# Optimization experiments

Measured on AMD Instinct MI355X. Metric: run time of the kernel, lower is better.

## Reference

```python
import jax, jax.numpy as jnp
import numpy as np

def setup_inputs() -> dict:
    key = jax.random.key(0)
    k1, k2, k3 = jax.random.split(key, 3)
    input_dim, hidden_dim = 512, 1024
    batch, seq_len = 32, 1024
    fan_in = input_dim + hidden_dim
    bound = 1.0 / np.sqrt(fan_in)
    x = jax.random.normal(k1, (batch, seq_len, input_dim), dtype=jnp.float32)
    # nn.Linear(input_dim+hidden_dim, 4*hidden_dim): weight [4H, I+H], bias [4H]
    W = jax.random.uniform(k2, (4 * hidden_dim, fan_in), minval=-bound, maxval=bound, dtype=jnp.float32)
    b = jax.random.uniform(k3, (4 * hidden_dim,), minval=-bound, maxval=bound, dtype=jnp.float32)
    return {"x": x, "W": W, "b": b}

def reference(x, W, b):
    B, T, I = x.shape
    H4 = W.shape[0]
    H = H4 // 4
    # Split weight into input and hidden parts (concat(x, h) @ W.T == x @ Wx.T + h @ Wh.T)
    Wx = W[:, :I]   # [4H, I]
    Wh = W[:, I:]   # [4H, H]
    # Precompute input contribution for all timesteps in one GEMM
    xW = jnp.einsum('bti,gi->btg', x, Wx) + b  # [B, T, 4H]

    def step(carry, xw_t):
        h, c = carry
        gates = xw_t + h @ Wh.T  # [B, 4H]
        i_t, f_t, g_t, o_t = jnp.split(gates, 4, axis=1)
        i_t = jax.nn.sigmoid(i_t)
        f_t = jax.nn.sigmoid(f_t)
        g_t = jnp.tanh(g_t)
        o_t = jax.nn.sigmoid(o_t)
        c_new = f_t * c + i_t * g_t
        h_new = o_t * jnp.tanh(c_new)
        return (h_new, c_new), h_new

    h0 = jnp.zeros((B, H), dtype=x.dtype)
    c0 = jnp.zeros((B, H), dtype=x.dtype)
    (_, _), hs = jax.lax.scan(step, (h0, c0), jnp.swapaxes(xW, 0, 1))  # hs: [T, B, H]
    return jnp.swapaxes(hs, 0, 1)  # [B, T, H]
```

## Files before the change

kernel.cpp:

```cpp
#include <hip/hip_runtime.h>
#include <cstdint>

#define BB 32
#define TT 1024
#define II 512
#define HH 1024
#define NTHREADS 512
#define NBLOCKS  256

__device__ __forceinline__ float sigm(float v) { return 1.0f / (1.0f + __expf(-v)); }
__device__ __forceinline__ float mytanh(float v) {
  float e = __expf(2.0f * v);
  return (e - 1.0f) / (e + 1.0f);
}

__global__ __launch_bounds__(NTHREADS, 2)
void lstm_step(const float* __restrict__ x, const float* __restrict__ W,
               const float* __restrict__ bias, const float* __restrict__ h_in,
               float* __restrict__ h_out, float* __restrict__ c_state,
               float* __restrict__ out, int t)
{
  __shared__ __align__(16) float sm[BB * HH];
  const int tid   = threadIdx.x;
  const int wave  = tid >> 6;
  const int lane  = tid & 63;
  const int ul    = wave >> 1;
  const int u     = blockIdx.x * 4 + ul;
  const int bbase = (wave & 1) * 16;

  float wreg[4][24];
  float bias4[4];
  #pragma unroll
  for (int q = 0; q < 4; ++q) {
    const float* wr = W + (size_t)(q * HH + u) * (II + HH);
    #pragma unroll
    for (int j = 0; j < 24; ++j) wreg[q][j] = wr[lane + 64 * j];
    bias4[q] = bias[q * HH + u];
  }

  float acc[16][4];
  #pragma unroll
  for (int bl = 0; bl < 16; ++bl)
    #pragma unroll
    for (int q = 0; q < 4; ++q) acc[bl][q] = 0.0f;

  for (int idx = tid; idx < BB * II / 4; idx += NTHREADS) {
    const int b  = idx >> 7;
    const int ii = idx & 127;
    reinterpret_cast<float4*>(sm)[idx] =
        reinterpret_cast<const float4*>(x + (size_t)b * TT * II + (size_t)t * II)[ii];
  }
  __syncthreads();

  #pragma unroll
  for (int bl = 0; bl < 16; ++bl) {
    const float* row = sm + (bbase + bl) * II;
    float xv[8];
    #pragma unroll
    for (int j = 0; j < 8; ++j) xv[j] = row[lane + 64 * j];
    #pragma unroll
    for (int q = 0; q < 4; ++q)
      #pragma unroll
      for (int j = 0; j < 8; ++j) acc[bl][q] = fmaf(xv[j], wreg[q][j], acc[bl][q]);
  }
  __syncthreads();

  for (int idx = tid; idx < BB * HH / 4; idx += NTHREADS)
    reinterpret_cast<float4*>(sm)[idx] = reinterpret_cast<const float4*>(h_in)[idx];
  __syncthreads();

  #pragma unroll
  for (int bl = 0; bl < 16; ++bl) {
    const float* row = sm + (bbase + bl) * HH;
    float hv[16];
    #pragma unroll
    for (int j = 0; j < 16; ++j) hv[j] = row[lane + 64 * j];
    #pragma unroll
    for (int q = 0; q < 4; ++q)
      #pragma unroll
      for (int j = 0; j < 16; ++j) acc[bl][q] = fmaf(hv[j], wreg[q][8 + j], acc[bl][q]);
  }

  float g4[4] = {0.f, 0.f, 0.f, 0.f};
  #pragma unroll
  for (int bl = 0; bl < 16; ++bl) {
    float a0 = acc[bl][0], a1 = acc[bl][1], a2 = acc[bl][2], a3 = acc[bl][3];
    #pragma unroll
    for (int off = 32; off; off >>= 1) {
      a0 += __shfl_xor(a0, off, 64);
      a1 += __shfl_xor(a1, off, 64);
      a2 += __shfl_xor(a2, off, 64);
      a3 += __shfl_xor(a3, off, 64);
    }
    if (lane == bl) { g4[0] = a0; g4[1] = a1; g4[2] = a2; g4[3] = a3; }
  }

  if (lane < 16) {
    const int b = bbase + lane;
    const float gi = sigm(g4[0] + bias4[0]);
    const float gf = sigm(g4[1] + bias4[1]);
    const float gg = mytanh(g4[2] + bias4[2]);
    const float go = sigm(g4[3] + bias4[3]);
    const int ci = b * HH + u;
    const float cn = gf * c_state[ci] + gi * gg;
    c_state[ci] = cn;
    const float hn = go * mytanh(cn);
    h_out[ci] = hn;
    out[(size_t)b * TT * HH + (size_t)t * HH + u] = hn;
  }
}

extern "C" void kernel_launch(void* const* d_in, const int* in_sizes, int n_in,
                              void* d_out, int out_size, void* d_ws, size_t ws_size,
                              hipStream_t stream)
{
  const float* x = (const float*)d_in[0];
  const float* W = (const float*)d_in[1];
  const float* b = (const float*)d_in[2];
  float* out = (float*)d_out;

  float* h0 = (float*)d_ws;
  float* h1 = h0 + BB * HH;
  float* c  = h1 + BB * HH;
  hipMemsetAsync(d_ws, 0, (size_t)3 * BB * HH * sizeof(float), stream);

  for (int t = 0; t < TT; ++t) {
    const float* hin = (t & 1) ? h1 : h0;
    float*      hout = (t & 1) ? h0 : h1;
    lstm_step<<<NBLOCKS, NTHREADS, 0, stream>>>(x, W, b, hin, hout, c, out, t);
  }
}
```

Before: 24.24 ms.

## Replace per-timestep launches with persistent cooperative kernel using grid barrier

Turns the 1024 separate step launches into one cooperative persistent kernel. Blocks synchronise through a global atomic barrier between timesteps and keep weights and the cell state in registers. The previous h is read back from the output tensor into LDS with direct global-to-LDS loads, double-buffered with the next x slice. A transpose-style shuffle reduction has each lane hold one gate, removing the per-batch reduction loops. This removes launch overhead and weight reloads per step, at the cost of a spin barrier and a dependence on all 256 blocks being co-resident.

```diff
diff --git a/kernel.cpp b/kernel.cpp
--- a/kernel.cpp
+++ b/kernel.cpp
@@ -5,108 +5,186 @@
 #define TT 1024
 #define II 512
 #define HH 1024
+#define KK 1536
 #define NTHREADS 512
 #define NBLOCKS  256
 
-__device__ __forceinline__ float sigm(float v) { return 1.0f / (1.0f + __expf(-v)); }
-__device__ __forceinline__ float mytanh(float v) {
-  float e = __expf(2.0f * v);
-  return (e - 1.0f) / (e + 1.0f);
+__device__ __forceinline__ void gload16(const void* g, void* l) {
+  __builtin_amdgcn_global_load_lds(
+      (const __attribute__((address_space(1))) unsigned int*)g,
+      (__attribute__((address_space(3))) unsigned int*)l, 16, 0, 0);
+}
+
+__device__ __forceinline__ void grid_barrier(unsigned* bar) {
+  __syncthreads();
+  if (threadIdx.x == 0) {
+    __threadfence();
+    unsigned g = __hip_atomic_load(bar + 1, __ATOMIC_RELAXED, __HIP_MEMORY_SCOPE_AGENT);
+    unsigned old = __hip_atomic_fetch_add(bar, 1u, __ATOMIC_ACQ_REL, __HIP_MEMORY_SCOPE_AGENT);
+    if (old == NBLOCKS - 1) {
+      __hip_atomic_store(bar, 0u, __ATOMIC_RELAXED, __HIP_MEMORY_SCOPE_AGENT);
+      __hip_atomic_fetch_add(bar + 1, 1u, __ATOMIC_RELEASE, __HIP_MEMORY_SCOPE_AGENT);
+    } else {
+      while (__hip_atomic_load(bar + 1, __ATOMIC_ACQUIRE, __HIP_MEMORY_SCOPE_AGENT) == g)
+        __builtin_amdgcn_s_sleep(1);
+    }
+    __threadfence();
+  }
+  __syncthreads();
 }
 
 __global__ __launch_bounds__(NTHREADS, 2)
-void lstm_step(const float* __restrict__ x, const float* __restrict__ W,
-               const float* __restrict__ bias, const float* __restrict__ h_in,
-               float* __restrict__ h_out, float* __restrict__ c_state,
-               float* __restrict__ out, int t)
+void lstm_persist(const float* __restrict__ x, const float* __restrict__ W,
+                  const float* __restrict__ bias, float* __restrict__ out,
+                  unsigned* __restrict__ bar)
 {
-  __shared__ __align__(16) float sm[BB * HH];
+  __shared__ __align__(16) float smA[BB * II];
+  __shared__ __align__(16) float smB[BB * II];
+
   const int tid   = threadIdx.x;
+  const int lane  = tid & 63;
   const int wave  = tid >> 6;
-  const int lane  = tid & 63;
-  const int ul    = wave >> 1;
-  const int u     = blockIdx.x * 4 + ul;
+  const int u     = blockIdx.x * 4 + (wave >> 1);
   const int bbase = (wave & 1) * 16;
-
-  float wreg[4][24];
-  float bias4[4];
+  const int g4    = lane >> 2;
+  const int q     = lane & 3;
+
+  float wr[4][24];
   #pragma unroll
-  for (int q = 0; q < 4; ++q) {
-    const float* wr = W + (size_t)(q * HH + u) * (II + HH);
-    #pragma unroll
-    for (int j = 0; j < 24; ++j) wreg[q][j] = wr[lane + 64 * j];
-    bias4[q] = bias[q * HH + u];
-  }
-
-  float acc[16][4];
+  for (int r = 0; r < 4; ++r) {
+    const int qq = q ^ r;
+    const float* row = W + (size_t)(qq * HH + u) * KK;
+    #pragma unroll
+    for (int j = 0; j < 2; ++j) {
+      float4 v = *(const float4*)(row + 4 * lane + 256 * j);
+      wr[r][4*j+0] = v.x; wr[r][4*j+1] = v.y; wr[r][4*j+2] = v.z; wr[r][4*j+3] = v.w;
+    }
+    #pragma unroll
+    for (int j = 0; j < 4; ++j) {
+      float4 v = *(const float4*)(row + 512 + 4 * lane + 256 * j);
+      wr[r][8+4*j+0] = v.x; wr[r][8+4*j+1] = v.y; wr[r][8+4*j+2] = v.z; wr[r][8+4*j+3] = v.w;
+    }
+  }
+  const float bmine = bias[q * HH + u];
+  float c_reg = 0.0f;
+
   #pragma unroll
-  for (int bl = 0; bl < 16; ++bl)
-    #pragma unroll
-    for (int q = 0; q < 4; ++q) acc[bl][q] = 0.0f;
-
-  for (int idx = tid; idx < BB * II / 4; idx += NTHREADS) {
-    const int b  = idx >> 7;
-    const int ii = idx & 127;
-    reinterpret_cast<float4*>(sm)[idx] =
-        reinterpret_cast<const float4*>(x + (size_t)b * TT * II + (size_t)t * II)[ii];
+  for (int it = 0; it < 8; ++it) {
+    int idx = it * NTHREADS + tid;
+    int b = idx >> 7, c4 = idx & 127;
+    gload16(x + (size_t)b * TT * II + 4 * c4, smA + 4 * idx);
   }
   __syncthreads();
 
-  #pragma unroll
-  for (int bl = 0; bl < 16; ++bl) {
-    const float* row = sm + (bbase + bl) * II;
-    float xv[8];
-    #pragma unroll
-    for (int j = 0; j < 8; ++j) xv[j] = row[lane + 64 * j];
-    #pragma unroll
-    for (int q = 0; q < 4; ++q)
-      #pragma unroll
-      for (int j = 0; j < 8; ++j) acc[bl][q] = fmaf(xv[j], wreg[q][j], acc[bl][q]);
-  }
-  __syncthreads();
-
-  for (int idx = tid; idx < BB * HH / 4; idx += NTHREADS)
-    reinterpret_cast<float4*>(sm)[idx] = reinterpret_cast<const float4*>(h_in)[idx];
-  __syncthreads();
-
-  #pragma unroll
-  for (int bl = 0; bl < 16; ++bl) {
-    const float* row = sm + (bbase + bl) * HH;
-    float hv[16];
-    #pragma unroll
-    for (int j = 0; j < 16; ++j) hv[j] = row[lane + 64 * j];
-    #pragma unroll
-    for (int q = 0; q < 4; ++q)
-      #pragma unroll
-      for (int j = 0; j < 16; ++j) acc[bl][q] = fmaf(hv[j], wreg[q][8 + j], acc[bl][q]);
-  }
-
-  float g4[4] = {0.f, 0.f, 0.f, 0.f};
-  #pragma unroll
-  for (int bl = 0; bl < 16; ++bl) {
-    float a0 = acc[bl][0], a1 = acc[bl][1], a2 = acc[bl][2], a3 = acc[bl][3];
-    #pragma unroll
-    for (int off = 32; off; off >>= 1) {
-      a0 += __shfl_xor(a0, off, 64);
-      a1 += __shfl_xor(a1, off, 64);
-      a2 += __shfl_xor(a2, off, 64);
-      a3 += __shfl_xor(a3, off, 64);
-    }
-    if (lane == bl) { g4[0] = a0; g4[1] = a1; g4[2] = a2; g4[3] = a3; }
-  }
-
-  if (lane < 16) {
-    const int b = bbase + lane;
-    const float gi = sigm(g4[0] + bias4[0]);
-    const float gf = sigm(g4[1] + bias4[1]);
-    const float gg = mytanh(g4[2] + bias4[2]);
-    const float go = sigm(g4[3] + bias4[3]);
-    const int ci = b * HH + u;
-    const float cn = gf * c_state[ci] + gi * gg;
-    c_state[ci] = cn;
-    const float hn = go * mytanh(cn);
-    h_out[ci] = hn;
-    out[(size_t)b * TT * HH + (size_t)t * HH + u] = hn;
+  float acc[64];
+
+  #pragma unroll 1
+  for (int t = 0; t < TT; ++t) {
+    #pragma unroll
+    for (int i = 0; i < 64; ++i) acc[i] = 0.0f;
+
+    if (t > 0) {
+      grid_barrier(bar);
+      #pragma unroll
+      for (int it = 0; it < 8; ++it) {
+        int idx = it * NTHREADS + tid;
+        int b = idx >> 7, c4 = idx & 127;
+        gload16(out + (size_t)b * TT * HH + (size_t)(t - 1) * HH + 4 * c4, smB + 4 * idx);
+      }
+    }
+
+    #pragma unroll
+    for (int m = 0; m < 16; ++m) {
+      const int bl = bbase + (g4 ^ m);
+      const float4* Ar = (const float4*)(smA + bl * II);
+      float4 a0 = Ar[lane], a1 = Ar[lane + 64];
+      #pragma unroll
+      for (int r = 0; r < 4; ++r) {
+        float s = acc[4*m+r];
+        s = fmaf(a0.x, wr[r][0], s); s = fmaf(a0.y, wr[r][1], s);
+        s = fmaf(a0.z, wr[r][2], s); s = fmaf(a0.w, wr[r][3], s);
+        s = fmaf(a1.x, wr[r][4], s); s = fmaf(a1.y, wr[r][5], s);
+        s = fmaf(a1.z, wr[r][6], s); s = fmaf(a1.w, wr[r][7], s);
+        acc[4*m+r] = s;
+      }
+    }
+
+    if (t > 0) {
+      __syncthreads();
+      #pragma unroll
+      for (int it = 0; it < 8; ++it) {
+        int idx = it * NTHREADS + tid;
+        int b = idx >> 7, c4 = idx & 127;
+        gload16(out + (size_t)b * TT * HH + (size_t)(t - 1) * HH + 512 + 4 * c4, smA + 4 * idx);
+      }
+
+      #pragma unroll
+      for (int m = 0; m < 16; ++m) {
+        const int bl = bbase + (g4 ^ m);
+        const float4* Br = (const float4*)(smB + bl * II);
+        float4 h0 = Br[lane], h1 = Br[lane + 64];
+        #pragma unroll
+        for (int r = 0; r < 4; ++r) {
+          float s = acc[4*m+r];
+          s = fmaf(h0.x, wr[r][ 8], s); s = fmaf(h0.y, wr[r][ 9], s);
+          s = fmaf(h0.z, wr[r][10], s); s = fmaf(h0.w, wr[r][11], s);
+          s = fmaf(h1.x, wr[r][12], s); s = fmaf(h1.y, wr[r][13], s);
+          s = fmaf(h1.z, wr[r][14], s); s = fmaf(h1.w, wr[r][15], s);
+          acc[4*m+r] = s;
+        }
+      }
+
+      __syncthreads();
+      #pragma unroll
+      for (int m = 0; m < 16; ++m) {
+        const int bl = bbase + (g4 ^ m);
+        const float4* Ar = (const float4*)(smA + bl * II);
+        float4 h2 = Ar[lane], h3 = Ar[lane + 64];
+        #pragma unroll
+        for (int r = 0; r < 4; ++r) {
+          float s = acc[4*m+r];
+          s = fmaf(h2.x, wr[r][16], s); s = fmaf(h2.y, wr[r][17], s);
+          s = fmaf(h2.z, wr[r][18], s); s = fmaf(h2.w, wr[r][19], s);
+          s = fmaf(h3.x, wr[r][20], s); s = fmaf(h3.y, wr[r][21], s);
+          s = fmaf(h3.z, wr[r][22], s); s = fmaf(h3.w, wr[r][23], s);
+          acc[4*m+r] = s;
+        }
+      }
+    }
+
+    #pragma unroll
+    for (int half = 32; half >= 1; half >>= 1) {
+      #pragma unroll
+      for (int i = 0; i < half; ++i)
+        acc[i] += __shfl_xor(acc[i + half], half, 64);
+    }
+
+    {
+      float gv = acc[0] + bmine;
+      float y  = (q == 2) ? 2.0f * gv : gv;
+      float sg = 1.0f / (1.0f + __expf(-y));
+      float act = (q == 2) ? 2.0f * sg - 1.0f : sg;
+      float r2 = __shfl_xor(act, 2, 64);
+      float p  = (q == 1) ? act * c_reg : act * r2;
+      float r1 = __shfl_xor(p, 1, 64);
+      float cn = p + r1;
+      float so = 1.0f / (1.0f + __expf(-2.0f * cn));
+      float hv = r2 * (2.0f * so - 1.0f);
+      if (q == 1) {
+        c_reg = cn;
+        out[(size_t)(bbase + g4) * (TT * HH) + (size_t)t * HH + u] = hv;
+      }
+    }
+
+    if (t + 1 < TT) {
+      __syncthreads();
+      #pragma unroll
+      for (int it = 0; it < 8; ++it) {
+        int idx = it * NTHREADS + tid;
+        int b = idx >> 7, c4 = idx & 127;
+        gload16(x + (size_t)b * TT * II + (size_t)(t + 1) * II + 4 * c4, smA + 4 * idx);
+      }
+    }
   }
 }
 
@@ -118,15 +196,11 @@
   const float* W = (const float*)d_in[1];
   const float* b = (const float*)d_in[2];
   float* out = (float*)d_out;
-
-  float* h0 = (float*)d_ws;
-  float* h1 = h0 + BB * HH;
-  float* c  = h1 + BB * HH;
-  hipMemsetAsync(d_ws, 0, (size_t)3 * BB * HH * sizeof(float), stream);
-
-  for (int t = 0; t < TT; ++t) {
-    const float* hin = (t & 1) ? h1 : h0;
-    float*      hout = (t & 1) ? h0 : h1;
-    lstm_step<<<NBLOCKS, NTHREADS, 0, stream>>>(x, W, b, hin, hout, c, out, t);
-  }
-}
+  unsigned* bar = (unsigned*)d_ws;
+
+  hipMemsetAsync(d_ws, 0, 2 * sizeof(unsigned), stream);
+
+  void* args[] = { (void*)&x, (void*)&W, (void*)&b, (void*)&out, (void*)&bar };
+  hipLaunchCooperativeKernel((const void*)lstm_persist,
+                             dim3(NBLOCKS), dim3(NTHREADS), args, 0, stream);
+}
```

New measurement: 54.55 ms. 2.25x slower.
